# Optimization experiments

Measured on AMD Instinct MI355X. Metric: run time of the kernel, lower is better.

The kernel has to match this reference:

```python
import jax, jax.numpy as jnp
import numpy as np

HEAD_NUM = 16
EMBED_DIM = 512


def setup_inputs() -> dict:
    key = jax.random.key(0)
    k1, k2, k3, k4, k5 = jax.random.split(key, 5)
    B, N, D = 8, 2048, EMBED_DIM
    x = jax.random.normal(k1, (B, N, D), dtype=jnp.float32)
    dis_matrix = jax.random.uniform(k2, (B, N, N), dtype=jnp.float32)
    s = 1.0 / np.sqrt(D)
    Wq = jax.random.normal(k3, (D, D), dtype=jnp.float32) * s
    Wk = jax.random.normal(k4, (D, D), dtype=jnp.float32) * s
    Wv = jax.random.normal(k5, (D, D), dtype=jnp.float32) * s
    alpha = jnp.float32(1.0)
    return {"x": x, "dis_matrix": dis_matrix, "Wq": Wq, "Wk": Wk, "Wv": Wv, "alpha": alpha}


def _split_heads(t, H):
    # [B, N, D] -> [B, H, N, D//H]
    B, N, D = t.shape
    return t.reshape(B, N, H, D // H).transpose(0, 2, 1, 3)


def reference(x, dis_matrix, Wq, Wk, Wv, alpha):
    B, N, D = x.shape
    H = HEAD_NUM
    # nn.Linear(bias=False): y = x @ W.T
    q = _split_heads(x @ Wq.T, H)  # [B,H,N,dk]
    k = _split_heads(x @ Wk.T, H)
    v = _split_heads(x @ Wv.T, H)
    log2n = jnp.float32(np.log2(N))
    dis_weight = jnp.exp(-alpha * log2n * dis_matrix)  # [B,N,N]
    k_weight = jnp.exp(k)
    # contract over source node i -> target node j
    weight_1 = jnp.einsum('bij,bhik->bhjk', dis_weight, k_weight * v)
    weight_2 = jnp.einsum('bij,bhik->bhjk', dis_weight, k_weight)
    out = jax.nn.sigmoid(q) * (weight_1 / weight_2)  # [B,H,N,dk]
    return out.transpose(0, 2, 1, 3).reshape(B, N, D)
```

## Files before the change

kernel.cpp:

```cpp
#include <hip/hip_runtime.h>
#include <math.h>
#include <stdint.h>


typedef __bf16 bf16_t;
typedef __attribute__((ext_vector_type(4))) __bf16 bf16x4;
typedef __attribute__((ext_vector_type(8))) __bf16 bf16x8;
typedef __attribute__((ext_vector_type(4))) float f32x4;

#define MFMA_BF16(a, b, c) __builtin_amdgcn_mfma_f32_16x16x32_bf16((a), (b), (c), 0, 0, 0)

static __device__ __forceinline__ void async_ld16(const bf16_t* g, bf16_t* lds) {
  __builtin_amdgcn_global_load_lds(
      reinterpret_cast<__attribute__((address_space(1))) unsigned int*>(
          reinterpret_cast<uintptr_t>(g)),
      reinterpret_cast<__attribute__((address_space(3))) unsigned int*>(
          reinterpret_cast<uintptr_t>(lds)),
      16, 0, 0);
}

#define WAITV(N)                                          \
  do {                                                    \
    asm volatile("s_waitcnt vmcnt(" #N ")" ::: "memory"); \
    __builtin_amdgcn_sched_barrier(0);                    \
  } while (0)

template <int ROWS>
static __device__ __forceinline__ void stage3(const bf16_t* g, int ldg, bf16_t* lds,
                                              int wv, int lane) {
  const int r_in = lane >> 3;
  const int cpos = lane & 7;
#pragma unroll
  for (int s = 0; s < ROWS / 32; ++s) {
    int rbase = wv * (ROWS / 4) + s * 8;
    int row = rbase + r_in;
    int cg = cpos ^ (row & 7);
    async_ld16(g + (size_t)row * ldg + cg * 8, lds + rbase * 64 + lane * 8);
  }
}

static __device__ __forceinline__ bf16x8 frag3(const bf16_t* lds, int row16,
                                               int l15, int quad, int kc) {
  int p = (quad | (kc << 2)) ^ (l15 & 7);
  return *(const bf16x8*)&lds[(row16 + l15) * 64 + p * 8];
}

__global__ __launch_bounds__(256) void cvt_all(const float* __restrict__ x,
                                               const float* __restrict__ wq,
                                               const float* __restrict__ wk,
                                               const float* __restrict__ wv,
                                               bf16_t* __restrict__ xb,
                                               bf16_t* __restrict__ wall) {
  int i = blockIdx.x * 256 + threadIdx.x;
  if (i >= 2293760) return;
  const float* src;
  bf16_t* dst;
  int off;
  if (i < 2097152) {
    src = x; dst = xb; off = i;
  } else {
    int j = i - 2097152;
    int sel = j >> 16;
    off = j & 65535;
    src = (sel == 0) ? wq : (sel == 1) ? wk : wv;
    dst = wall + (size_t)sel * 262144;
  }
  f32x4 f = ((const f32x4*)src)[off];
  bf16x4 o;
  o[0] = (bf16_t)f[0]; o[1] = (bf16_t)f[1]; o[2] = (bf16_t)f[2]; o[3] = (bf16_t)f[3];
  ((bf16x4*)dst)[off] = o;
}

__global__ __launch_bounds__(256, 4) void proj_dw(const bf16_t* __restrict__ A,
                                                  const bf16_t* __restrict__ W,
                                                  bf16_t* __restrict__ qs,
                                                  bf16_t* __restrict__ kwT,
                                                  bf16_t* __restrict__ kwvT,
                                                  const float* __restrict__ dis,
                                                  bf16_t* __restrict__ dwT,
                                                  const float* __restrict__ alpha) {
  __shared__ __align__(16) char pool[32768];
  const int tid = threadIdx.x;
  const int idx = blockIdx.x;
  const int g19 = idx / 19, r19 = idx % 19;

  if (r19 >= 3) {
    int sub = g19 * 16 + (r19 - 3);
    int jt = sub & 31, it = (sub >> 5) & 31, b = sub >> 10;
    bf16_t* t = (bf16_t*)pool;
    const float coef = -alpha[0] * 11.0f;
    const int j0 = jt * 64, i0 = it * 64;
    const int rr = tid >> 4, cc = (tid & 15) * 4;
#pragma unroll
    for (int p = 0; p < 4; ++p) {
      int i = rr + p * 16;
      f32x4 d = *(const f32x4*)&dis[((size_t)(b * 2048 + i0 + i)) * 2048 + j0 + cc];
#pragma unroll
      for (int e = 0; e < 4; ++e) t[(cc + e) * 65 + i] = (bf16_t)__expf(coef * d[e]);
    }
    __syncthreads();
#pragma unroll
    for (int p = 0; p < 4; ++p) {
      int j = rr + p * 16;
      bf16x4 o;
#pragma unroll
      for (int e = 0; e < 4; ++e) o[e] = t[j * 65 + cc + e];
      *(bf16x4*)&dwT[((size_t)(b * 2048 + j0 + j)) * 2048 + i0 + cc] = o;
    }
    return;
  }

  const int sub = g19 * 3 + r19;
  const int m_blk = sub / 12, n_blk = sub % 12;
  bf16_t* As = (bf16_t*)pool;
  const int K = 512;
  const int wv = tid >> 6, lane = tid & 63;
  const int l15 = lane & 15, quad = lane >> 4;
  const int wm = wv >> 1, wn = wv & 1;
  const bf16_t* Am = A + (size_t)(m_blk * 128) * K;
  const int b = m_blk >> 4;

  if (n_blk < 4) {
    bf16_t* Bsq = (bf16_t*)(pool + 16384);
    const int c_loc = n_blk * 128;
    f32x4 acc[4][4];
#pragma unroll
    for (int a = 0; a < 4; ++a)
#pragma unroll
      for (int c = 0; c < 4; ++c) acc[a][c] = (f32x4){0.f, 0.f, 0.f, 0.f};

    for (int k0 = 0; k0 < K; k0 += 64) {
      stage3<128>(Am + k0, K, As, wv, lane);
      stage3<128>(W + (size_t)c_loc * K + k0, K, Bsq, wv, lane);
      __syncthreads();
#pragma unroll
      for (int kc = 0; kc < 2; ++kc) {
        bf16x8 a[4], bb[4];
#pragma unroll
        for (int mf = 0; mf < 4; ++mf) a[mf] = frag3(As, wm * 64 + mf * 16, l15, quad, kc);
#pragma unroll
        for (int nf = 0; nf < 4; ++nf) bb[nf] = frag3(Bsq, wn * 64 + nf * 16, l15, quad, kc);
#pragma unroll
        for (int mf = 0; mf < 4; ++mf)
#pragma unroll
          for (int nf = 0; nf < 4; ++nf) acc[mf][nf] = MFMA_BF16(a[mf], bb[nf], acc[mf][nf]);
      }
      __syncthreads();
    }
#pragma unroll
    for (int mf = 0; mf < 4; ++mf)
#pragma unroll
      for (int nf = 0; nf < 4; ++nf) {
        int j16 = (m_blk & 15) * 8 + wm * 4 + mf;
        int c16 = n_blk * 8 + wn * 4 + nf;
        bf16x4 o;
#pragma unroll
        for (int r = 0; r < 4; ++r)
          o[r] = (bf16_t)(1.0f / (1.0f + __expf(-acc[mf][nf][r])));
        size_t off = (((size_t)b * 128 + j16) * 32 + c16) * 256 + quad * 64 + l15 * 4;
        *(bf16x4*)&qs[off] = o;
      }
  } else {
    bf16_t* Bk = (bf16_t*)(pool + 16384);
    bf16_t* Bv = (bf16_t*)(pool + 24576);
    const int c_loc = (n_blk - 4) * 64;
    f32x4 acck[4][2], accv[4][2];
#pragma unroll
    for (int a = 0; a < 4; ++a)
#pragma unroll
      for (int c = 0; c < 2; ++c) {
        acck[a][c] = (f32x4){0.f, 0.f, 0.f, 0.f};
        accv[a][c] = (f32x4){0.f, 0.f, 0.f, 0.f};
      }
    const bf16_t* Wk = W + (size_t)(512 + c_loc) * K;
    const bf16_t* Wv = W + (size_t)(1024 + c_loc) * K;

    for (int k0 = 0; k0 < K; k0 += 64) {
      stage3<128>(Am + k0, K, As, wv, lane);
      stage3<64>(Wk + k0, K, Bk, wv, lane);
      stage3<64>(Wv + k0, K, Bv, wv, lane);
      __syncthreads();
#pragma unroll
      for (int kc = 0; kc < 2; ++kc) {
        bf16x8 a[4], bk[2], bv[2];
#pragma unroll
        for (int mf = 0; mf < 4; ++mf) a[mf] = frag3(As, wm * 64 + mf * 16, l15, quad, kc);
#pragma unroll
        for (int nf = 0; nf < 2; ++nf) {
          bk[nf] = frag3(Bk, wn * 32 + nf * 16, l15, quad, kc);
          bv[nf] = frag3(Bv, wn * 32 + nf * 16, l15, quad, kc);
        }
#pragma unroll
        for (int mf = 0; mf < 4; ++mf)
#pragma unroll
          for (int nf = 0; nf < 2; ++nf) {
            acck[mf][nf] = MFMA_BF16(a[mf], bk[nf], acck[mf][nf]);
            accv[mf][nf] = MFMA_BF16(a[mf], bv[nf], accv[mf][nf]);
          }
      }
      __syncthreads();
    }

    bf16_t* Lk = (bf16_t*)pool;
    bf16_t* Lv = (bf16_t*)(pool + 8704);
    const int t0 = (m_blk * 128) & 2047;
#pragma unroll
    for (int ci = 0; ci < 2; ++ci) {
      if (wn == ci) {
#pragma unroll
        for (int mf = 0; mf < 4; ++mf)
#pragma unroll
          for (int nf = 0; nf < 2; ++nf) {
            int cl = nf * 16 + l15;
            int tl = wm * 64 + mf * 16 + quad * 4;
#pragma unroll
            for (int r = 0; r < 4; ++r) {
              float kw = __expf(acck[mf][nf][r]);
              Lk[cl * 136 + tl + r] = (bf16_t)kw;
              Lv[cl * 136 + tl + r] = (bf16_t)(kw * accv[mf][nf][r]);
            }
          }
      }
      __syncthreads();
      {
        int rowt = tid >> 3, colt = (tid & 7) * 16;
        int c = c_loc + ci * 32 + rowt;
        size_t g = ((size_t)b * 512 + c) * 2048 + t0 + colt;
        *(bf16x8*)&kwT[g] = *(const bf16x8*)&Lk[rowt * 136 + colt];
        *(bf16x8*)&kwT[g + 8] = *(const bf16x8*)&Lk[rowt * 136 + colt + 8];
        *(bf16x8*)&kwvT[g] = *(const bf16x8*)&Lv[rowt * 136 + colt];
        *(bf16x8*)&kwvT[g + 8] = *(const bf16x8*)&Lv[rowt * 136 + colt + 8];
      }
      __syncthreads();
    }
  }
}

__global__ __launch_bounds__(512, 2) void main_gemm(const bf16_t* __restrict__ dwT,
                                                    const bf16_t* __restrict__ kwvT,
                                                    const bf16_t* __restrict__ kwT,
                                                    const bf16_t* __restrict__ qs,
                                                    float* __restrict__ out) {
  extern __shared__ __align__(16) char smem_raw[];
  bf16_t* const lds = (bf16_t*)smem_raw;
  const int K = 2048;
  const int tid = threadIdx.x;
  const int wv = tid >> 6, lane = tid & 63;
  const int l15 = lane & 15, quad = lane >> 4;
  const int bi = blockIdx.x;
  const int b = bi & 7, nbb = (bi >> 3) & 3, mb = bi >> 5;
  const int wm = wv >> 2, wn = wv & 3;
  const int r_in = lane >> 3, cpos = lane & 7;
  const int cg = cpos ^ r_in;

  const bf16_t* const Ab = dwT + ((size_t)b * 2048 + mb * 256) * K;
  const bf16_t* const BvB = kwvT + (size_t)b * 512 * K;
  const bf16_t* const BkB = kwT + (size_t)b * 512 * K;

  const bf16_t* aSrc[4];
  int aDst[4];
#pragma unroll
  for (int s = 0; s < 4; ++s) {
    const int row = s * 64 + wv * 8 + r_in;
    aSrc[s] = Ab + (size_t)row * K + cg * 8;
    aDst[s] = s * 4096 + wv * 512 + lane * 8;
  }
  const bf16_t* bSrc[4];
  int bDst[4];
#pragma unroll
  for (int cb = 0; cb < 4; ++cb) {
    const int base1 = (cb & 1) * 128 + (cb >> 1) * 32;
    const int rowbase = base1 + (wv >> 2) * 64 + (wv & 3) * 8;
    const int row = rowbase + r_in;
    const int type = (row >> 4) & 1;
    const int crow = nbb * 128 + (row >> 5) * 16 + (row & 15);
    bSrc[cb] = (type ? BkB : BvB) + (size_t)crow * K + cg * 8;
    bDst[cb] = 16384 + rowbase * 64 + lane * 8;
  }

  f32x4 acc[8][4];
#pragma unroll
  for (int m = 0; m < 8; ++m)
#pragma unroll
    for (int n = 0; n < 4; ++n) acc[m][n] = (f32x4){0.f, 0.f, 0.f, 0.f};

  bf16x8 a[8];
  bf16x8 b0[4];
  bf16x8 b1[4];

#define STAGE_A(dst, s, koff) async_ld16(aSrc[s] + (koff), lds + (dst)*32768 + aDst[s])
#define STAGE_B(dst, cb, koff) async_ld16(bSrc[cb] + (koff), lds + (dst)*32768 + bDst[cb])

#define LOADA(As_, mh)                                                             \
  do {                                                                             \
    _Pragma("unroll") for (int mf = 0; mf < 4; ++mf)                               \
        _Pragma("unroll") for (int kc = 0; kc < 2; ++kc)                           \
            a[mf * 2 + kc] =                                                       \
        frag3((As_), wm * 128 + (mh)*64 + mf * 16, l15, quad, kc);                 \
  } while (0)

#define LOADB(Bs_, dstarr, nh)                                                     \
  do {                                                                             \
    _Pragma("unroll") for (int nf = 0; nf < 2; ++nf)                               \
        _Pragma("unroll") for (int kc = 0; kc < 2; ++kc)                           \
            dstarr[nf * 2 + kc] =                                                  \
        frag3((Bs_), wn * 64 + (nh)*32 + nf * 16, l15, quad, kc);                  \
  } while (0)

#define MFMA_PH(mh, nh, barr)                                                      \
  do {                                                                             \
    __builtin_amdgcn_s_setprio(1);                                                 \
    _Pragma("unroll") for (int kc = 0; kc < 2; ++kc)                               \
        _Pragma("unroll") for (int mf = 0; mf < 4; ++mf)                           \
            _Pragma("unroll") for (int nf = 0; nf < 2; ++nf)                       \
                acc[(mh)*4 + mf][(nh)*2 + nf] =                                    \
        MFMA_BF16(a[mf * 2 + kc], barr[nf * 2 + kc], acc[(mh)*4 + mf][(nh)*2 + nf]); \
    __builtin_amdgcn_s_setprio(0);                                                 \
  } while (0)

  STAGE_A(0, 0, 0); STAGE_A(0, 2, 0); STAGE_B(0, 0, 0); STAGE_B(0, 1, 0);
  STAGE_B(0, 2, 0); STAGE_B(0, 3, 0); STAGE_A(0, 1, 0); STAGE_A(0, 3, 0);
  WAITV(4);
  __builtin_amdgcn_s_barrier();

  for (int t = 0; t < 32; ++t) {
    const int c = t & 1;
    const int nx = c ^ 1;
    const bf16_t* As_c = lds + c * 32768;
    const bf16_t* Bs_c = As_c + 16384;
    const int ko = (t + 1) * 64;
    if (t < 31) { STAGE_A(nx, 0, ko); STAGE_A(nx, 2, ko); STAGE_B(nx, 0, ko); STAGE_B(nx, 1, ko); }
    LOADA(As_c, 0);
    LOADB(Bs_c, b0, 0);
    __builtin_amdgcn_s_barrier();
    MFMA_PH(0, 0, b0);
    WAITV(6);
    __builtin_amdgcn_s_barrier();
    if (t < 31) { STAGE_B(nx, 2, ko); STAGE_B(nx, 3, ko); }
    LOADB(Bs_c, b1, 1);
    __builtin_amdgcn_s_barrier();
    MFMA_PH(0, 1, b1);
    WAITV(6);
    __builtin_amdgcn_s_barrier();
    if (t < 31) { STAGE_A(nx, 1, ko); STAGE_A(nx, 3, ko); }
    LOADA(As_c, 1);
    __builtin_amdgcn_s_barrier();
    MFMA_PH(1, 1, b1);
    __builtin_amdgcn_s_barrier();
    MFMA_PH(1, 0, b0);
    if (t < 30) {
      WAITV(4);
      __builtin_amdgcn_s_barrier();
    } else if (t == 30) {
      WAITV(0);
      __builtin_amdgcn_s_barrier();
    }
  }

#undef STAGE_A
#undef STAGE_B
#undef LOADA
#undef LOADB
#undef MFMA_PH

#pragma unroll
  for (int mf = 0; mf < 8; ++mf)
#pragma unroll
    for (int p = 0; p < 2; ++p) {
      f32x4 w1 = acc[mf][2 * p];
      f32x4 w2 = acc[mf][2 * p + 1];
      const int j16 = mb * 16 + wm * 8 + mf;
      const int c16 = nbb * 8 + wn * 2 + p;
      size_t qoff = (((size_t)b * 128 + j16) * 32 + c16) * 256 + quad * 64 + l15 * 4;
      bf16x4 qv = *(const bf16x4*)&qs[qoff];
      const int ccol = c16 * 16 + l15;
#pragma unroll
      for (int r = 0; r < 4; ++r) {
        const int j = j16 * 16 + quad * 4 + r;
        out[((size_t)b * 2048 + j) * 512 + ccol] = (float)qv[r] * (w1[r] / w2[r]);
      }
    }
}

extern "C" void kernel_launch(void* const* d_in, const int* in_sizes, int n_in,
                              void* d_out, int out_size, void* d_ws, size_t ws_size,
                              hipStream_t stream) {
  const float* x = (const float*)d_in[0];
  const float* dis = (const float*)d_in[1];
  const float* Wq = (const float*)d_in[2];
  const float* Wk = (const float*)d_in[3];
  const float* Wv = (const float*)d_in[4];
  const float* alpha = (const float*)d_in[5];
  float* out = (float*)d_out;

  char* p = (char*)d_ws;
  bf16_t* x_bf = (bf16_t*)p;  p += (size_t)16384 * 512 * 2;
  bf16_t* Wall = (bf16_t*)p;  p += (size_t)1536 * 512 * 2;
  bf16_t* kwT  = (bf16_t*)p;  p += (size_t)8 * 512 * 2048 * 2;
  bf16_t* kwvT = (bf16_t*)p;  p += (size_t)8 * 512 * 2048 * 2;
  bf16_t* dwT  = (bf16_t*)p;  p += (size_t)8 * 2048 * 2048 * 2;
  bf16_t* qs_bf = (bf16_t*)p; p += (size_t)16384 * 512 * 2;
  if ((size_t)(p - (char*)d_ws) > ws_size) return;

  static bool attr_done = false;
  if (!attr_done) {
    hipFuncSetAttribute(reinterpret_cast<const void*>(main_gemm),
                        hipFuncAttributeMaxDynamicSharedMemorySize, 131072);
    attr_done = true;
  }

  cvt_all<<<8960, 256, 0, stream>>>(x, Wq, Wk, Wv, x_bf, Wall);
  proj_dw<<<9728, 256, 0, stream>>>(x_bf, Wall, qs_bf, kwT, kwvT, dis, dwT, alpha);
  main_gemm<<<256, 512, 131072, stream>>>(dwT, kwvT, kwT, qs_bf, out);
}
```

Before: 308.6 us.

## Fuse distance-weight exp and transpose into main GEMM A-operand staging

Removes the separate pass that computed exp(-alpha*log2N*dis), transposed it and wrote a bf16 dwT buffer. The main GEMM now loads fp32 dis tiles into registers, applies exp, converts to bf16 and writes them swizzled into LDS as the A operand. This cuts a full write and reread of a 64MB intermediate and drops most of the proj_dw launch. In exchange, the GEMM does register-staged loads, exp work and extra synchronisation inside its pipeline. Each block also reads fp32 data, twice the bytes of the old bf16 A tile, which may stall the MFMA pipeline.

```diff
diff --git a/kernel.cpp b/kernel.cpp
--- a/kernel.cpp
+++ b/kernel.cpp
@@ -17,6 +17,12 @@
       reinterpret_cast<__attribute__((address_space(3))) unsigned int*>(
           reinterpret_cast<uintptr_t>(lds)),
       16, 0, 0);
+}
+
+static __device__ __forceinline__ f32x4 async_ldg_f32x4(const float* p) {
+  f32x4 r;
+  asm volatile("global_load_dwordx4 %0, %1, off" : "=&v"(r) : "v"(p) : "memory");
+  return r;
 }
 
 #define WAITV(N)                                          \
@@ -75,42 +81,10 @@
                                                   const bf16_t* __restrict__ W,
                                                   bf16_t* __restrict__ qs,
                                                   bf16_t* __restrict__ kwT,
-                                                  bf16_t* __restrict__ kwvT,
-                                                  const float* __restrict__ dis,
-                                                  bf16_t* __restrict__ dwT,
-                                                  const float* __restrict__ alpha) {
+                                                  bf16_t* __restrict__ kwvT) {
   __shared__ __align__(16) char pool[32768];
   const int tid = threadIdx.x;
-  const int idx = blockIdx.x;
-  const int g19 = idx / 19, r19 = idx % 19;
-
-  if (r19 >= 3) {
-    int sub = g19 * 16 + (r19 - 3);
-    int jt = sub & 31, it = (sub >> 5) & 31, b = sub >> 10;
-    bf16_t* t = (bf16_t*)pool;
-    const float coef = -alpha[0] * 11.0f;
-    const int j0 = jt * 64, i0 = it * 64;
-    const int rr = tid >> 4, cc = (tid & 15) * 4;
-#pragma unroll
-    for (int p = 0; p < 4; ++p) {
-      int i = rr + p * 16;
-      f32x4 d = *(const f32x4*)&dis[((size_t)(b * 2048 + i0 + i)) * 2048 + j0 + cc];
-#pragma unroll
-      for (int e = 0; e < 4; ++e) t[(cc + e) * 65 + i] = (bf16_t)__expf(coef * d[e]);
-    }
-    __syncthreads();
-#pragma unroll
-    for (int p = 0; p < 4; ++p) {
-      int j = rr + p * 16;
-      bf16x4 o;
-#pragma unroll
-      for (int e = 0; e < 4; ++e) o[e] = t[j * 65 + cc + e];
-      *(bf16x4*)&dwT[((size_t)(b * 2048 + j0 + j)) * 2048 + i0 + cc] = o;
-    }
-    return;
-  }
-
-  const int sub = g19 * 3 + r19;
+  const int sub = blockIdx.x;
   const int m_blk = sub / 12, n_blk = sub % 12;
   bf16_t* As = (bf16_t*)pool;
   const int K = 512;
@@ -236,10 +210,11 @@
   }
 }
 
-__global__ __launch_bounds__(512, 2) void main_gemm(const bf16_t* __restrict__ dwT,
+__global__ __launch_bounds__(512, 2) void main_gemm(const float* __restrict__ dis,
                                                     const bf16_t* __restrict__ kwvT,
                                                     const bf16_t* __restrict__ kwT,
                                                     const bf16_t* __restrict__ qs,
+                                                    const float* __restrict__ alpha,
                                                     float* __restrict__ out) {
   extern __shared__ __align__(16) char smem_raw[];
   bf16_t* const lds = (bf16_t*)smem_raw;
@@ -253,18 +228,14 @@
   const int r_in = lane >> 3, cpos = lane & 7;
   const int cg = cpos ^ r_in;
 
-  const bf16_t* const Ab = dwT + ((size_t)b * 2048 + mb * 256) * K;
+  const float coef = -alpha[0] * 11.0f;
+
   const bf16_t* const BvB = kwvT + (size_t)b * 512 * K;
   const bf16_t* const BkB = kwT + (size_t)b * 512 * K;
 
-  const bf16_t* aSrc[4];
-  int aDst[4];
-#pragma unroll
-  for (int s = 0; s < 4; ++s) {
-    const int row = s * 64 + wv * 8 + r_in;
-    aSrc[s] = Ab + (size_t)row * K + cg * 8;
-    aDst[s] = s * 4096 + wv * 512 + lane * 8;
-  }
+  const int jb = tid >> 3, ib = tid & 7;
+  const float* const disB = dis + (size_t)b * 2048 * 2048 + (size_t)(mb * 256 + jb * 4);
+
   const bf16_t* bSrc[4];
   int bDst[4];
 #pragma unroll
@@ -287,9 +258,24 @@
   bf16x8 a[8];
   bf16x8 b0[4];
   bf16x8 b1[4];
-
-#define STAGE_A(dst, s, koff) async_ld16(aSrc[s] + (koff), lds + (dst)*32768 + aDst[s])
+  f32x4 rA0[4], rA1[4];
+
 #define STAGE_B(dst, cb, koff) async_ld16(bSrc[cb] + (koff), lds + (dst)*32768 + bDst[cb])
+
+#define CONVW(dstbuf, h, rr)                                                     \
+  do {                                                                           \
+    bf16_t* An_ = lds + (dstbuf)*32768;                                          \
+    const int il_ = (h)*32 + ib * 4;                                             \
+    _Pragma("unroll") for (int cc_ = 0; cc_ < 4; ++cc_) {                        \
+      const int jl_ = jb * 4 + cc_;                                              \
+      bf16x4 w_;                                                                 \
+      w_[0] = (bf16_t)__expf(coef * (rr)[0][cc_]);                               \
+      w_[1] = (bf16_t)__expf(coef * (rr)[1][cc_]);                               \
+      w_[2] = (bf16_t)__expf(coef * (rr)[2][cc_]);                               \
+      w_[3] = (bf16_t)__expf(coef * (rr)[3][cc_]);                               \
+      *(bf16x4*)&An_[jl_ * 64 + (((il_ >> 3) ^ (jl_ & 7)) << 3) + (il_ & 4)] = w_; \
+    }                                                                            \
+  } while (0)
 
 #define LOADA(As_, mh)                                                             \
   do {                                                                             \
@@ -318,47 +304,51 @@
     __builtin_amdgcn_s_setprio(0);                                                 \
   } while (0)
 
-  STAGE_A(0, 0, 0); STAGE_A(0, 2, 0); STAGE_B(0, 0, 0); STAGE_B(0, 1, 0);
-  STAGE_B(0, 2, 0); STAGE_B(0, 3, 0); STAGE_A(0, 1, 0); STAGE_A(0, 3, 0);
-  WAITV(4);
-  __builtin_amdgcn_s_barrier();
+  STAGE_B(0, 0, 0); STAGE_B(0, 1, 0); STAGE_B(0, 2, 0); STAGE_B(0, 3, 0);
+#pragma unroll
+  for (int r = 0; r < 4; ++r) rA0[r] = async_ldg_f32x4(disB + (size_t)(ib * 4 + r) * 2048);
+#pragma unroll
+  for (int r = 0; r < 4; ++r) rA1[r] = async_ldg_f32x4(disB + (size_t)(32 + ib * 4 + r) * 2048);
+  WAITV(0);
+  CONVW(0, 0, rA0);
+  CONVW(0, 1, rA1);
+  __syncthreads();
 
   for (int t = 0; t < 32; ++t) {
     const int c = t & 1;
     const int nx = c ^ 1;
     const bf16_t* As_c = lds + c * 32768;
     const bf16_t* Bs_c = As_c + 16384;
-    const int ko = (t + 1) * 64;
-    if (t < 31) { STAGE_A(nx, 0, ko); STAGE_A(nx, 2, ko); STAGE_B(nx, 0, ko); STAGE_B(nx, 1, ko); }
+    if (t < 31) {
+      const int ko = (t + 1) * 64;
+      STAGE_B(nx, 0, ko); STAGE_B(nx, 1, ko); STAGE_B(nx, 2, ko); STAGE_B(nx, 3, ko);
+      const float* dp = disB + (size_t)(t + 1) * 64 * 2048;
+#pragma unroll
+      for (int r = 0; r < 4; ++r) rA0[r] = async_ldg_f32x4(dp + (size_t)(ib * 4 + r) * 2048);
+#pragma unroll
+      for (int r = 0; r < 4; ++r) rA1[r] = async_ldg_f32x4(dp + (size_t)(32 + ib * 4 + r) * 2048);
+    }
     LOADA(As_c, 0);
     LOADB(Bs_c, b0, 0);
     __builtin_amdgcn_s_barrier();
     MFMA_PH(0, 0, b0);
-    WAITV(6);
-    __builtin_amdgcn_s_barrier();
-    if (t < 31) { STAGE_B(nx, 2, ko); STAGE_B(nx, 3, ko); }
+    __builtin_amdgcn_s_barrier();
     LOADB(Bs_c, b1, 1);
     __builtin_amdgcn_s_barrier();
     MFMA_PH(0, 1, b1);
-    WAITV(6);
-    __builtin_amdgcn_s_barrier();
-    if (t < 31) { STAGE_A(nx, 1, ko); STAGE_A(nx, 3, ko); }
+    __builtin_amdgcn_s_barrier();
+    if (t < 31) { WAITV(4); CONVW(nx, 0, rA0); }
     LOADA(As_c, 1);
     __builtin_amdgcn_s_barrier();
     MFMA_PH(1, 1, b1);
     __builtin_amdgcn_s_barrier();
+    if (t < 31) { WAITV(0); CONVW(nx, 1, rA1); }
     MFMA_PH(1, 0, b0);
-    if (t < 30) {
-      WAITV(4);
-      __builtin_amdgcn_s_barrier();
-    } else if (t == 30) {
-      WAITV(0);
-      __builtin_amdgcn_s_barrier();
-    }
-  }
-
-#undef STAGE_A
+    __syncthreads();
+  }
+
 #undef STAGE_B
+#undef CONVW
 #undef LOADA
 #undef LOADB
 #undef MFMA_PH
@@ -398,7 +388,6 @@
   bf16_t* Wall = (bf16_t*)p;  p += (size_t)1536 * 512 * 2;
   bf16_t* kwT  = (bf16_t*)p;  p += (size_t)8 * 512 * 2048 * 2;
   bf16_t* kwvT = (bf16_t*)p;  p += (size_t)8 * 512 * 2048 * 2;
-  bf16_t* dwT  = (bf16_t*)p;  p += (size_t)8 * 2048 * 2048 * 2;
   bf16_t* qs_bf = (bf16_t*)p; p += (size_t)16384 * 512 * 2;
   if ((size_t)(p - (char*)d_ws) > ws_size) return;
 
@@ -410,6 +399,6 @@
   }
 
   cvt_all<<<8960, 256, 0, stream>>>(x, Wq, Wk, Wv, x_bf, Wall);
-  proj_dw<<<9728, 256, 0, stream>>>(x_bf, Wall, qs_bf, kwT, kwvT, dis, dwT, alpha);
-  main_gemm<<<256, 512, 131072, stream>>>(dwT, kwvT, kwT, qs_bf, out);
-}
+  proj_dw<<<1536, 256, 0, stream>>>(x_bf, Wall, qs_bf, kwT, kwvT);
+  main_gemm<<<256, 512, 131072, stream>>>(dis, kwvT, kwT, qs_bf, alpha, out);
+}
```

Result: slower. 379.4 us (+22.9%).
